# Kernel tuning notes

Measured on AMD Instinct MI355X. Metric: run time of the kernel, lower is better.

## Reference

```python
import jax, jax.numpy as jnp
import numpy as np

TOKENS, D_IN, D_OUT = 16384, 2048, 2048


def setup_inputs() -> dict:
    key = jax.random.key(0)
    k1, k2, k3 = jax.random.split(key, 3)
    x = jax.random.normal(k1, (TOKENS, D_IN), dtype=jnp.float32)
    # int8 quantized weight, stored transposed as [in_features, out_features]
    weight = jax.random.randint(k2, (D_IN, D_OUT), -128, 128).astype(jnp.int8)
    # per-output-channel dequant scale, shape [1, out_features]
    scale = (jax.random.uniform(k3, (1, D_OUT), dtype=jnp.float32) * 0.01 + 1e-4)
    return {"x": x, "scale": scale, "weight": weight}


def reference(x, scale, weight):
    # x: [N, in], weight: int8 [in, out] (pre-transposed), scale: [1, out]
    tokens = x.shape[:-1]
    xf = x.reshape(-1, x.shape[-1])
    # cast int8 weight to activation dtype, dense matmul, per-channel scale
    y = jnp.matmul(xf, weight.astype(x.dtype)) * scale
    # bias path is dead in the original (`if self.bias:` on a tensor); omitted
    return y.reshape(tokens + (weight.shape[-1],))
```

## Files before the change

### kernel.cpp

```cpp
#include <hip/hip_runtime.h>
#include <cstdint>


#define M_TOK 16384
#define K_DIM 2048
#define N_DIM 2048
#define BK 32

typedef _Float16 f16;
typedef f16 f16x4 __attribute__((ext_vector_type(4)));
typedef f16 f16x8 __attribute__((ext_vector_type(8)));
typedef float f32x4 __attribute__((ext_vector_type(4)));

__global__ void convert_x_kernel(const float* __restrict__ x, f16* __restrict__ xh) {
  const int n4 = (M_TOK * K_DIM) / 4;
  const int stride = gridDim.x * blockDim.x;
  for (int i = blockIdx.x * blockDim.x + threadIdx.x; i < n4; i += stride) {
    float4 v = ((const float4*)x)[i];
    f16x4 h;
    h[0] = (f16)v.x; h[1] = (f16)v.y; h[2] = (f16)v.z; h[3] = (f16)v.w;
    ((f16x4*)xh)[i] = h;
  }
}

__global__ void convert_w_kernel(const int* __restrict__ w, f16* __restrict__ wt) {
  __shared__ f16 tile[64][68];
  const int tid = threadIdx.x;
  const int nb = blockIdx.x * 64;
  const int kb = blockIdx.y * 64;
  const int cq = tid & 15;
  const int rr = tid >> 4;

#pragma unroll
  for (int g = 0; g < 4; ++g) {
    int krow = g * 16 + rr;
    const int* p = w + (size_t)(kb + krow) * N_DIM + nb + cq * 4;
    int4 v = *(const int4*)p;
    tile[cq * 4 + 0][krow] = (f16)(float)v.x;
    tile[cq * 4 + 1][krow] = (f16)(float)v.y;
    tile[cq * 4 + 2][krow] = (f16)(float)v.z;
    tile[cq * 4 + 3][krow] = (f16)(float)v.w;
  }
  __syncthreads();
#pragma unroll
  for (int g = 0; g < 4; ++g) {
    int nrow = g * 16 + rr;
    f16x4 o;
#pragma unroll
    for (int j = 0; j < 4; ++j)
      o[j] = tile[nrow][cq * 4 + j];
    *(f16x4*)(wt + (size_t)(nb + nrow) * K_DIM + kb + cq * 4) = o;
  }
}

__device__ __forceinline__ void async_load16(const void* g, void* l) {
  __builtin_amdgcn_global_load_lds((__attribute__((address_space(1))) void*)g,
                                   (__attribute__((address_space(3))) void*)l,
                                   16, 0, 0);
}

__global__ __launch_bounds__(256) void gemm_f16(
    const f16* __restrict__ xh, const f16* __restrict__ wt,
    const float* __restrict__ scale, float* __restrict__ out) {
  __shared__ __align__(16) f16 sA[128 * BK];
  __shared__ __align__(16) f16 sB[128 * BK];

  const int tid = threadIdx.x;
  const int wave = tid >> 6;
  const int lane = tid & 63;
  const int m0 = blockIdx.y * 128;
  const int n0 = blockIdx.x * 128;
  const int wm = (wave & 1) * 64;
  const int wn = (wave >> 1) * 64;

  const int c0 = wave * 2;
  const int rowA = c0 * 16 + (lane >> 2);
  const int kq8 = (lane & 3) * 8;

  const f16* gA0 = xh + (size_t)(m0 + rowA) * K_DIM + kq8;
  const f16* gA1 = xh + (size_t)(m0 + rowA + 16) * K_DIM + kq8;
  const f16* gB0 = wt + (size_t)(n0 + rowA) * K_DIM + kq8;
  const f16* gB1 = wt + (size_t)(n0 + rowA + 16) * K_DIM + kq8;

  f16* lA0 = sA + c0 * 512;  f16* lA1 = lA0 + 512;
  f16* lB0 = sB + c0 * 512;  f16* lB1 = lB0 + 512;

  const int fr = lane & 15;
  const int fq = (lane >> 4) * 8;

  f32x4 acc[4][4] = {};

  for (int k0 = 0; k0 < K_DIM; k0 += BK) {
    async_load16(gA0 + k0, lA0);
    async_load16(gA1 + k0, lA1);
    async_load16(gB0 + k0, lB0);
    async_load16(gB1 + k0, lB1);
    __syncthreads();

    f16x8 a[4], b[4];
#pragma unroll
    for (int t = 0; t < 4; ++t) {
      a[t] = *(const f16x8*)&sA[(wm + t * 16 + fr) * BK + fq];
      b[t] = *(const f16x8*)&sB[(wn + t * 16 + fr) * BK + fq];
    }
#pragma unroll
    for (int mm = 0; mm < 4; ++mm)
#pragma unroll
      for (int nn = 0; nn < 4; ++nn)
        acc[mm][nn] = __builtin_amdgcn_mfma_f32_16x16x32_f16(a[mm], b[nn], acc[mm][nn], 0, 0, 0);
    __syncthreads();
  }

#pragma unroll
  for (int nn = 0; nn < 4; ++nn) {
    int col = n0 + wn + nn * 16 + fr;
    float s = scale[col];
#pragma unroll
    for (int mm = 0; mm < 4; ++mm) {
      int rbase = m0 + wm + mm * 16 + (lane >> 4) * 4;
      f32x4 v = acc[mm][nn];
#pragma unroll
      for (int r = 0; r < 4; ++r)
        out[(size_t)(rbase + r) * N_DIM + col] = v[r] * s;
    }
  }
}

extern "C" void kernel_launch(void* const* d_in, const int* in_sizes, int n_in,
                              void* d_out, int out_size, void* d_ws, size_t ws_size,
                              hipStream_t stream) {
  const float* x     = (const float*)d_in[0];
  const float* scale = (const float*)d_in[1];
  const int* w       = (const int*)d_in[2];
  float* out         = (float*)d_out;

  char* ws = (char*)d_ws;
  f16* xh = (f16*)ws;
  f16* wt = (f16*)(ws + (size_t)M_TOK * K_DIM * 2);

  convert_x_kernel<<<8192, 256, 0, stream>>>(x, xh);
  convert_w_kernel<<<dim3(N_DIM / 64, K_DIM / 64), 256, 0, stream>>>(w, wt);
  gemm_f16<<<dim3(N_DIM / 128, M_TOK / 128), 256, 0, stream>>>(xh, wt, scale, out);
}
```

Baseline: 393.4 us.

## Switch GEMM to 32x32x16 MFMA with XOR-swizzled LDS layout

```diff
diff --git a/kernel.cpp b/kernel.cpp
--- a/kernel.cpp
+++ b/kernel.cpp
@@ -10,16 +10,18 @@
 typedef _Float16 f16;
 typedef f16 f16x4 __attribute__((ext_vector_type(4)));
 typedef f16 f16x8 __attribute__((ext_vector_type(8)));
-typedef float f32x4 __attribute__((ext_vector_type(4)));
+typedef float f32x16 __attribute__((ext_vector_type(16)));
 
 __global__ void convert_x_kernel(const float* __restrict__ x, f16* __restrict__ xh) {
-  const int n4 = (M_TOK * K_DIM) / 4;
+  const int n8 = (M_TOK * K_DIM) / 8;
   const int stride = gridDim.x * blockDim.x;
-  for (int i = blockIdx.x * blockDim.x + threadIdx.x; i < n4; i += stride) {
-    float4 v = ((const float4*)x)[i];
-    f16x4 h;
-    h[0] = (f16)v.x; h[1] = (f16)v.y; h[2] = (f16)v.z; h[3] = (f16)v.w;
-    ((f16x4*)xh)[i] = h;
+  for (int i = blockIdx.x * blockDim.x + threadIdx.x; i < n8; i += stride) {
+    float4 v0 = ((const float4*)x)[i * 2];
+    float4 v1 = ((const float4*)x)[i * 2 + 1];
+    f16x8 h;
+    h[0] = (f16)v0.x; h[1] = (f16)v0.y; h[2] = (f16)v0.z; h[3] = (f16)v0.w;
+    h[4] = (f16)v1.x; h[5] = (f16)v1.y; h[6] = (f16)v1.z; h[7] = (f16)v1.w;
+    ((f16x8*)xh)[i] = h;
   }
 }
 
@@ -47,8 +49,7 @@
     int nrow = g * 16 + rr;
     f16x4 o;
 #pragma unroll
-    for (int j = 0; j < 4; ++j)
-      o[j] = tile[nrow][cq * 4 + j];
+    for (int j = 0; j < 4; ++j) o[j] = tile[nrow][cq * 4 + j];
     *(f16x4*)(wt + (size_t)(nb + nrow) * K_DIM + kb + cq * 4) = o;
   }
 }
@@ -73,22 +74,33 @@
   const int wm = (wave & 1) * 64;
   const int wn = (wave >> 1) * 64;
 
-  const int c0 = wave * 2;
-  const int rowA = c0 * 16 + (lane >> 2);
-  const int kq8 = (lane & 3) * 8;
+  const int q0 = wave * 2;
+  const int rowS = q0 * 16 + (lane >> 2);
+  const int cS = (lane & 3) ^ ((rowS >> 1) & 3);
+  const f16* gA0 = xh + (size_t)(m0 + rowS) * K_DIM + cS * 8;
+  const f16* gA1 = gA0 + (size_t)16 * K_DIM;
+  const f16* gB0 = wt + (size_t)(n0 + rowS) * K_DIM + cS * 8;
+  const f16* gB1 = gB0 + (size_t)16 * K_DIM;
+  f16* lA0 = sA + q0 * 512;  f16* lA1 = lA0 + 512;
+  f16* lB0 = sB + q0 * 512;  f16* lB1 = lB0 + 512;
 
-  const f16* gA0 = xh + (size_t)(m0 + rowA) * K_DIM + kq8;
-  const f16* gA1 = xh + (size_t)(m0 + rowA + 16) * K_DIM + kq8;
-  const f16* gB0 = wt + (size_t)(n0 + rowA) * K_DIM + kq8;
-  const f16* gB1 = wt + (size_t)(n0 + rowA + 16) * K_DIM + kq8;
+  const int fr = lane & 31;
+  const int kq = lane >> 5;
+  const f16* aAddr[2][2];
+  const f16* bAddr[2][2];
+#pragma unroll
+  for (int mt = 0; mt < 2; ++mt)
+#pragma unroll
+    for (int kh = 0; kh < 2; ++kh) {
+      int rA = wm + mt * 32 + fr;
+      int rB = wn + mt * 32 + fr;
+      int cA = (kh * 2 + kq) ^ ((rA >> 1) & 3);
+      int cB = (kh * 2 + kq) ^ ((rB >> 1) & 3);
+      aAddr[mt][kh] = sA + rA * BK + cA * 8;
+      bAddr[mt][kh] = sB + rB * BK + cB * 8;
+    }
 
-  f16* lA0 = sA + c0 * 512;  f16* lA1 = lA0 + 512;
-  f16* lB0 = sB + c0 * 512;  f16* lB1 = lB0 + 512;
-
-  const int fr = lane & 15;
-  const int fq = (lane >> 4) * 8;
-
-  f32x4 acc[4][4] = {};
+  f32x16 acc[2][2] = {};
 
   for (int k0 = 0; k0 < K_DIM; k0 += BK) {
     async_load16(gA0 + k0, lA0);
@@ -97,31 +109,37 @@
     async_load16(gB1 + k0, lB1);
     __syncthreads();
 
-    f16x8 a[4], b[4];
+    f16x8 a[2][2], b[2][2];
 #pragma unroll
-    for (int t = 0; t < 4; ++t) {
-      a[t] = *(const f16x8*)&sA[(wm + t * 16 + fr) * BK + fq];
-      b[t] = *(const f16x8*)&sB[(wn + t * 16 + fr) * BK + fq];
-    }
+    for (int mt = 0; mt < 2; ++mt)
 #pragma unroll
-    for (int mm = 0; mm < 4; ++mm)
+      for (int kh = 0; kh < 2; ++kh) {
+        a[mt][kh] = *(const f16x8*)aAddr[mt][kh];
+        b[mt][kh] = *(const f16x8*)bAddr[mt][kh];
+      }
 #pragma unroll
-      for (int nn = 0; nn < 4; ++nn)
-        acc[mm][nn] = __builtin_amdgcn_mfma_f32_16x16x32_f16(a[mm], b[nn], acc[mm][nn], 0, 0, 0);
+    for (int kh = 0; kh < 2; ++kh)
+#pragma unroll
+      for (int mt = 0; mt < 2; ++mt)
+#pragma unroll
+        for (int nt = 0; nt < 2; ++nt)
+          acc[mt][nt] = __builtin_amdgcn_mfma_f32_32x32x16_f16(
+              a[mt][kh], b[nt][kh], acc[mt][nt], 0, 0, 0);
     __syncthreads();
   }
 
 #pragma unroll
-  for (int nn = 0; nn < 4; ++nn) {
-    int col = n0 + wn + nn * 16 + fr;
+  for (int nt = 0; nt < 2; ++nt) {
+    int col = n0 + wn + nt * 32 + fr;
     float s = scale[col];
 #pragma unroll
-    for (int mm = 0; mm < 4; ++mm) {
-      int rbase = m0 + wm + mm * 16 + (lane >> 4) * 4;
-      f32x4 v = acc[mm][nn];
+    for (int mt = 0; mt < 2; ++mt) {
+      int rbase = m0 + wm + mt * 32 + 4 * kq;
 #pragma unroll
-      for (int r = 0; r < 4; ++r)
-        out[(size_t)(rbase + r) * N_DIM + col] = v[r] * s;
+      for (int reg = 0; reg < 16; ++reg) {
+        int row = rbase + (reg & 3) + 8 * (reg >> 2);
+        out[(size_t)row * N_DIM + col] = acc[mt][nt][reg] * s;
+      }
     }
   }
 }
```

New measurement: 414.1 us. 5.3% more time.

## Load B fragments directly from global into registers with prefetch, fuse convert kernels

Applied to the files above, without the earlier changes.

```diff
diff --git a/kernel.cpp b/kernel.cpp
--- a/kernel.cpp
+++ b/kernel.cpp
@@ -12,44 +12,45 @@
 typedef f16 f16x8 __attribute__((ext_vector_type(8)));
 typedef float f32x4 __attribute__((ext_vector_type(4)));
 
-__global__ void convert_x_kernel(const float* __restrict__ x, f16* __restrict__ xh) {
-  const int n4 = (M_TOK * K_DIM) / 4;
-  const int stride = gridDim.x * blockDim.x;
-  for (int i = blockIdx.x * blockDim.x + threadIdx.x; i < n4; i += stride) {
-    float4 v = ((const float4*)x)[i];
-    f16x4 h;
-    h[0] = (f16)v.x; h[1] = (f16)v.y; h[2] = (f16)v.z; h[3] = (f16)v.w;
-    ((f16x4*)xh)[i] = h;
-  }
-}
-
-__global__ void convert_w_kernel(const int* __restrict__ w, f16* __restrict__ wt) {
-  __shared__ f16 tile[64][68];
+__global__ void convert_kernel(const float* __restrict__ x, const int* __restrict__ w,
+                               f16* __restrict__ xh, f16* __restrict__ wt) {
   const int tid = threadIdx.x;
-  const int nb = blockIdx.x * 64;
-  const int kb = blockIdx.y * 64;
-  const int cq = tid & 15;
-  const int rr = tid >> 4;
-
+  if (blockIdx.x < 1024) {
+    __shared__ f16 tile[64][68];
+    const int nb = (blockIdx.x & 31) * 64;
+    const int kb = (blockIdx.x >> 5) * 64;
+    const int cq = tid & 15;
+    const int rr = tid >> 4;
 #pragma unroll
-  for (int g = 0; g < 4; ++g) {
-    int krow = g * 16 + rr;
-    const int* p = w + (size_t)(kb + krow) * N_DIM + nb + cq * 4;
-    int4 v = *(const int4*)p;
-    tile[cq * 4 + 0][krow] = (f16)(float)v.x;
-    tile[cq * 4 + 1][krow] = (f16)(float)v.y;
-    tile[cq * 4 + 2][krow] = (f16)(float)v.z;
-    tile[cq * 4 + 3][krow] = (f16)(float)v.w;
-  }
-  __syncthreads();
+    for (int g = 0; g < 4; ++g) {
+      int krow = g * 16 + rr;
+      const int* p = w + (size_t)(kb + krow) * N_DIM + nb + cq * 4;
+      int4 v = *(const int4*)p;
+      tile[cq * 4 + 0][krow] = (f16)(float)v.x;
+      tile[cq * 4 + 1][krow] = (f16)(float)v.y;
+      tile[cq * 4 + 2][krow] = (f16)(float)v.z;
+      tile[cq * 4 + 3][krow] = (f16)(float)v.w;
+    }
+    __syncthreads();
 #pragma unroll
-  for (int g = 0; g < 4; ++g) {
-    int nrow = g * 16 + rr;
-    f16x4 o;
+    for (int g = 0; g < 4; ++g) {
+      int nrow = g * 16 + rr;
+      f16x4 o;
 #pragma unroll
-    for (int j = 0; j < 4; ++j)
-      o[j] = tile[nrow][cq * 4 + j];
-    *(f16x4*)(wt + (size_t)(nb + nrow) * K_DIM + kb + cq * 4) = o;
+      for (int j = 0; j < 4; ++j) o[j] = tile[nrow][cq * 4 + j];
+      *(f16x4*)(wt + (size_t)(nb + nrow) * K_DIM + kb + cq * 4) = o;
+    }
+  } else {
+    const int n8 = (M_TOK * K_DIM) / 8;
+    const int nthreads = 4096 * 256;
+    for (int i = (blockIdx.x - 1024) * 256 + tid; i < n8; i += nthreads) {
+      float4 v0 = ((const float4*)x)[i * 2];
+      float4 v1 = ((const float4*)x)[i * 2 + 1];
+      f16x8 h;
+      h[0] = (f16)v0.x; h[1] = (f16)v0.y; h[2] = (f16)v0.z; h[3] = (f16)v0.w;
+      h[4] = (f16)v1.x; h[5] = (f16)v1.y; h[6] = (f16)v1.z; h[7] = (f16)v1.w;
+      ((f16x8*)xh)[i] = h;
+    }
   }
 }
 
@@ -59,11 +60,10 @@
                                    16, 0, 0);
 }
 
-__global__ __launch_bounds__(256) void gemm_f16(
+__global__ __launch_bounds__(256, 4) void gemm_f16(
     const f16* __restrict__ xh, const f16* __restrict__ wt,
     const float* __restrict__ scale, float* __restrict__ out) {
   __shared__ __align__(16) f16 sA[128 * BK];
-  __shared__ __align__(16) f16 sB[128 * BK];
 
   const int tid = threadIdx.x;
   const int wave = tid >> 6;
@@ -76,38 +76,46 @@
   const int c0 = wave * 2;
   const int rowA = c0 * 16 + (lane >> 2);
   const int kq8 = (lane & 3) * 8;
-
   const f16* gA0 = xh + (size_t)(m0 + rowA) * K_DIM + kq8;
-  const f16* gA1 = xh + (size_t)(m0 + rowA + 16) * K_DIM + kq8;
-  const f16* gB0 = wt + (size_t)(n0 + rowA) * K_DIM + kq8;
-  const f16* gB1 = wt + (size_t)(n0 + rowA + 16) * K_DIM + kq8;
-
-  f16* lA0 = sA + c0 * 512;  f16* lA1 = lA0 + 512;
-  f16* lB0 = sB + c0 * 512;  f16* lB1 = lB0 + 512;
+  const f16* gA1 = gA0 + (size_t)16 * K_DIM;
+  f16* lA0 = sA + c0 * 512;
+  f16* lA1 = lA0 + 512;
 
   const int fr = lane & 15;
   const int fq = (lane >> 4) * 8;
 
+  const f16* gBf = wt + (size_t)(n0 + wn + fr) * K_DIM + fq;
+
   f32x4 acc[4][4] = {};
+  f16x8 bCur[4], bNext[4];
+#pragma unroll
+  for (int t = 0; t < 4; ++t)
+    bNext[t] = *(const f16x8*)(gBf + (size_t)t * 16 * K_DIM);
 
   for (int k0 = 0; k0 < K_DIM; k0 += BK) {
     async_load16(gA0 + k0, lA0);
     async_load16(gA1 + k0, lA1);
-    async_load16(gB0 + k0, lB0);
-    async_load16(gB1 + k0, lB1);
     __syncthreads();
 
-    f16x8 a[4], b[4];
+    f16x8 a[4];
 #pragma unroll
-    for (int t = 0; t < 4; ++t) {
+    for (int t = 0; t < 4; ++t)
       a[t] = *(const f16x8*)&sA[(wm + t * 16 + fr) * BK + fq];
-      b[t] = *(const f16x8*)&sB[(wn + t * 16 + fr) * BK + fq];
-    }
+
+#pragma unroll
+    for (int t = 0; t < 4; ++t) bCur[t] = bNext[t];
+
+    const int kpf = (k0 + BK) & (K_DIM - 1);
+#pragma unroll
+    for (int t = 0; t < 4; ++t)
+      bNext[t] = *(const f16x8*)(gBf + (size_t)t * 16 * K_DIM + kpf);
+
 #pragma unroll
     for (int mm = 0; mm < 4; ++mm)
 #pragma unroll
       for (int nn = 0; nn < 4; ++nn)
-        acc[mm][nn] = __builtin_amdgcn_mfma_f32_16x16x32_f16(a[mm], b[nn], acc[mm][nn], 0, 0, 0);
+        acc[mm][nn] = __builtin_amdgcn_mfma_f32_16x16x32_f16(a[mm], bCur[nn], acc[mm][nn], 0, 0, 0);
+
     __syncthreads();
   }
 
@@ -138,7 +146,6 @@
   f16* xh = (f16*)ws;
   f16* wt = (f16*)(ws + (size_t)M_TOK * K_DIM * 2);
 
-  convert_x_kernel<<<8192, 256, 0, stream>>>(x, xh);
-  convert_w_kernel<<<dim3(N_DIM / 64, K_DIM / 64), 256, 0, stream>>>(w, wt);
+  convert_kernel<<<5120, 256, 0, stream>>>(x, w, xh, wt);
   gemm_f16<<<dim3(N_DIM / 128, M_TOK / 128), 256, 0, stream>>>(xh, wt, scale, out);
 }
```

Measured after the change: 510.2 us. 29.7% more time.
